# Kernel tuning notes

Hardware: AMD Instinct MI355X
Metric: run time of the kernel (lower is better)

Reference implementation:

```python
import jax, jax.numpy as jnp
import numpy as np

B, N, D, FF, L = 32, 1000, 128, 512, 6
EPS = 1e-5  # InstanceNorm1d default eps


def _inorm(x, g, b):
    # InstanceNorm1d on [B, d, N] == normalize over sequence dim N per channel (biased var)
    m = jnp.mean(x, axis=1, keepdims=True)
    v = jnp.var(x, axis=1, keepdims=True)
    return (x - m) / jnp.sqrt(v + EPS) * g + b


def setup_inputs() -> dict:
    key = jax.random.key(0)
    ks = jax.random.split(key, 10)
    s = 0.05
    data = jax.random.normal(ks[0], (B, N, 2), dtype=jnp.float32)
    # negative pairwise distances (module calls it negative_dist)
    dist = -jax.random.uniform(ks[1], (B, N, N), dtype=jnp.float32)
    log_scale = jnp.ones((1,), dtype=jnp.float32)
    We = jax.random.normal(ks[2], (D, 2), dtype=jnp.float32) * s
    be = jnp.zeros((D,), dtype=jnp.float32)
    Wq = jax.random.normal(ks[3], (L, D, D), dtype=jnp.float32) * s
    Wk = jax.random.normal(ks[4], (L, D, D), dtype=jnp.float32) * s
    Wv = jax.random.normal(ks[5], (L, D, D), dtype=jnp.float32) * s
    g1 = jnp.ones((L, D), dtype=jnp.float32)
    b1 = jnp.zeros((L, D), dtype=jnp.float32)
    W1 = jax.random.normal(ks[6], (L, FF, D), dtype=jnp.float32) * s
    bw1 = jnp.zeros((L, FF), dtype=jnp.float32)
    W2 = jax.random.normal(ks[7], (L, D, FF), dtype=jnp.float32) * s
    bw2 = jnp.zeros((L, D), dtype=jnp.float32)
    g2 = jnp.ones((L, D), dtype=jnp.float32)
    b2 = jnp.zeros((L, D), dtype=jnp.float32)
    alpha = jnp.ones((L,), dtype=jnp.float32)  # AFT_dist_alpha per layer
    return dict(data=data, dist=dist, log_scale=log_scale, We=We, be=be,
                Wq=Wq, Wk=Wk, Wv=Wv, g1=g1, b1=b1, W1=W1, bw1=bw1,
                W2=W2, bw2=bw2, g2=g2, b2=b2, alpha=alpha)


def reference(data, dist, log_scale, We, be, Wq, Wk, Wv, g1, b1, W1, bw1, W2, bw2, g2, b2, alpha):
    x = data @ We.T + be  # [B,N,D]
    for i in range(L):
        q = x @ Wq[i].T
        k = x @ Wk[i].T
        v = x @ Wv[i].T
        A = jnp.exp(log_scale[0] * alpha[i] * dist)  # [B,N,N]
        ek = jnp.exp(k)
        bias = jnp.einsum('bnm,bmd->bnd', A, ek * v)
        denom = jnp.einsum('bnm,bmd->bnd', A, ek)
        out = jax.nn.sigmoid(q) * (bias / denom)
        x1 = _inorm(x + out, g1[i], b1[i])
        h = jax.nn.relu(x1 @ W1[i].T + bw1[i]) @ W2[i].T + bw2[i]
        x = _inorm(x1 + h, g2[i], b2[i])
    return x
```

## Files before the change

kernel.cpp:

```cpp
#include <hip/hip_runtime.h>
#include <hip/hip_bf16.h>

typedef __attribute__((ext_vector_type(4))) float f32x4;
typedef __attribute__((ext_vector_type(8))) short bf16x8;
typedef __attribute__((ext_vector_type(4))) short s16x4;

#define LCOUNT 6

static __device__ __forceinline__ unsigned short f2b(float f){
  __hip_bfloat16 h = __float2bfloat16(f);
  return __builtin_bit_cast(unsigned short, h);
}
static __device__ __forceinline__ float b2f(unsigned short u){
  unsigned int x = ((unsigned int)u) << 16;
  return __builtin_bit_cast(float, x);
}
static __device__ __forceinline__ void gl16(const void* g, void* l){
  __builtin_amdgcn_global_load_lds(
      (const __attribute__((address_space(1))) void*)g,
      (__attribute__((address_space(3))) void*)l, 16, 0, 0);
}
static __device__ __forceinline__ f32x4 mfma16(bf16x8 a, bf16x8 b, f32x4 c){
  return __builtin_amdgcn_mfma_f32_16x16x32_bf16(a, b, c, 0, 0, 0);
}

__global__ void k_cvt5(const float* __restrict__ Wq, const float* __restrict__ Wk,
                       const float* __restrict__ Wv, const float* __restrict__ W1,
                       const float* __restrict__ W2,
                       unsigned short* __restrict__ wqb, unsigned short* __restrict__ wkb,
                       unsigned short* __restrict__ wvb, unsigned short* __restrict__ w1b,
                       unsigned short* __restrict__ w2b){
  int i = blockIdx.x*256 + threadIdx.x;
  if (i < 98304) wqb[i] = f2b(Wq[i]);
  else if (i < 196608) wkb[i-98304] = f2b(Wk[i-98304]);
  else if (i < 294912) wvb[i-196608] = f2b(Wv[i-196608]);
  else if (i < 688128) w1b[i-294912] = f2b(W1[i-294912]);
  else w2b[i-688128] = f2b(W2[i-688128]);
}

__global__ void k_cvtdist(const float* __restrict__ dist, unsigned short* __restrict__ db){
  int t = blockIdx.x*256 + threadIdx.x;
  int row = t >> 7, ch = t & 127;
  bf16x8 w;
  if (ch >= 125){
#pragma unroll
    for (int e=0;e<8;e++) w[e] = 0;
  } else {
    const float* p = dist + (size_t)row*1000 + ch*8;
    f32x4 a = *(const f32x4*)p;
    f32x4 b = *(const f32x4*)(p + 4);
#pragma unroll
    for (int e=0;e<4;e++){ w[e] = (short)f2b(a[e]); w[4+e] = (short)f2b(b[e]); }
  }
  *(bf16x8*)&db[(size_t)row*1024 + ch*8] = w;
}

__global__ void k_embed(const float* __restrict__ data, const float* __restrict__ We,
                        const float* __restrict__ be, float* __restrict__ x,
                        unsigned short* __restrict__ xb){
  int idx = blockIdx.x*256 + threadIdx.x;
  int d = idx & 127, bn = idx >> 7;
  float v = data[bn*2]*We[d*2] + data[bn*2+1]*We[d*2+1] + be[d];
  x[idx] = v; xb[idx] = f2b(v);
}

__global__ __launch_bounds__(256) void k_napply(
  const float* __restrict__ src, const float* __restrict__ part, int cnt,
  const float* __restrict__ g, const float* __restrict__ beta,
  float* __restrict__ dstf, unsigned short* __restrict__ dstb,
  float* __restrict__ dout)
{
  __shared__ float sna[128], snc[128];
  int blk = blockIdx.x, tid = threadIdx.x;
  int b = blk / 125;
  if (tid < 128){
    float s1 = 0.f, s2 = 0.f;
    for (int c = 0; c < cnt; ++c){
      size_t pi = (((size_t)b*cnt + c)*128 + tid)*2;
      s1 += part[pi]; s2 += part[pi+1];
    }
    float mean = s1 * 1e-3f;
    float var  = s2 * 1e-3f - mean*mean;
    float a = g[tid] * rsqrtf(var + 1e-5f);
    sna[tid] = a; snc[tid] = beta[tid] - mean*a;
  }
  __syncthreads();
  size_t base = (size_t)blk*1024 + tid*4;
  f32x4 v = *(const f32x4*)&src[base];
  int d0 = (tid*4) & 127;
  f32x4 o; s16x4 ob;
#pragma unroll
  for (int e=0;e<4;e++){
    o[e] = v[e]*sna[d0+e] + snc[d0+e];
    ob[e] = (short)f2b(o[e]);
  }
  *(f32x4*)&dstf[base] = o;
  *(s16x4*)&dstb[base] = ob;
  if (dout) *(f32x4*)&dout[base] = o;
}

__global__ __launch_bounds__(256) void k_qkv(
  const unsigned short* __restrict__ xb,
  const unsigned short* __restrict__ Wqb, const unsigned short* __restrict__ Wkb,
  const unsigned short* __restrict__ Wvb,
  unsigned short* __restrict__ sigq, unsigned short* __restrict__ Zc)
{
  __shared__ unsigned short LA[2][4][64][8];
  __shared__ unsigned short LB[2][4][256][8];
  int tid = threadIdx.x, wid = tid>>6, lane = tid&63;
  int l15 = lane&15, lg = lane>>4;
  int wm = wid>>1, wn = wid&1;
  int bt = blockIdx.x, b = bt>>4, t = bt&15;
  int kv = blockIdx.y;
  int lrow = t*64 + lane; if (lrow > 999) lrow = 999;
  size_t arow = (size_t)(b*1000 + lrow);

  f32x4 zf = {0.f,0.f,0.f,0.f};
  f32x4 acc[2][4], acc2[2][4];
#pragma unroll
  for (int i=0;i<2;i++)
#pragma unroll
    for (int j=0;j<4;j++){ acc[i][j] = zf; acc2[i][j] = zf; }

  auto stage = [&](int kk, int buf){
    int k0 = kk*32;
    gl16(xb + arow*128 + k0 + wid*8, &LA[buf][wid][0][0]);
    if (kv == 0){
#pragma unroll
      for (int t2=0;t2<2;++t2){
        int e = wid + t2*4, g2 = e>>1, nb = e&1;
        gl16(Wqb + (size_t)(nb*64+lane)*128 + k0 + g2*8, &LB[buf][g2][nb*64][0]);
      }
    } else {
#pragma unroll
      for (int t2=0;t2<4;++t2){
        int e = wid + t2*4, g2 = e&3, nb = e>>2;
        const unsigned short* src = (nb < 2)
          ? Wkb + (size_t)(nb*64+lane)*128 + k0 + g2*8
          : Wvb + (size_t)((nb-2)*64+lane)*128 + k0 + g2*8;
        gl16(src, &LB[buf][g2][nb*64][0]);
      }
    }
  };
  auto compute = [&](int buf){
    bf16x8 af[2];
#pragma unroll
    for (int i=0;i<2;i++) af[i] = *(const bf16x8*)&LA[buf][lg][wm*32 + i*16 + l15][0];
#pragma unroll
    for (int j=0;j<4;j++){
      bf16x8 bq = *(const bf16x8*)&LB[buf][lg][wn*64 + j*16 + l15][0];
#pragma unroll
      for (int i=0;i<2;i++) acc[i][j] = mfma16(af[i], bq, acc[i][j]);
      if (kv){
        bf16x8 bv = *(const bf16x8*)&LB[buf][lg][128 + wn*64 + j*16 + l15][0];
#pragma unroll
        for (int i=0;i<2;i++) acc2[i][j] = mfma16(af[i], bv, acc2[i][j]);
      }
    }
  };

  stage(0, 0);
  __syncthreads();
  for (int kk = 0; kk < 4; ++kk){
    int buf = kk & 1;
    if (kk < 3) stage(kk+1, buf^1);
    compute(buf);
    __syncthreads();
  }

#pragma unroll
  for (int i=0;i<2;i++){
    int m4 = t*64 + wm*32 + i*16 + lg*4;
    if (m4 >= 1000) continue;
#pragma unroll
    for (int j=0;j<4;j++){
      int col = wn*64 + j*16 + l15;
      if (kv == 0){
#pragma unroll
        for (int r=0;r<4;r++)
          sigq[(size_t)(b*1000 + m4 + r)*128 + col] = f2b(1.f/(1.f + __expf(-acc[i][j][r])));
      } else {
        s16x4 pv, pk;
#pragma unroll
        for (int r=0;r<4;r++){
          float ek = __expf(acc[i][j][r]);
          pk[r] = (short)f2b(ek);
          pv[r] = (short)f2b(ek * acc2[i][j][r]);
        }
        size_t base = ((size_t)(b*128 + (m4>>3))*256 + col)*8 + ((m4>>2)&1)*4;
        *(s16x4*)&Zc[base] = pv;
        *(s16x4*)&Zc[base + 1024] = pk;
      }
    }
  }
}

template<int USE16>
__global__ __launch_bounds__(256) void k_attn(
  const float* __restrict__ dist, const unsigned short* __restrict__ db16,
  const unsigned short* __restrict__ Zc, const unsigned short* __restrict__ sigq,
  float* __restrict__ x, float* __restrict__ partA,
  const float* __restrict__ log_scale, const float* __restrict__ alpha, int layer)
{
  union SM {
    struct { unsigned short A[2][4][32][8]; unsigned short B[2][4][256][8]; } st;
    float den[32][128];
  };
  __shared__ SM sm;
  int tid = threadIdx.x, wid = tid>>6, lane = tid&63;
  int l15 = lane&15, lg = lane>>4;
  int bb = blockIdx.y, t = blockIdx.x, n0 = t*32;
  float sc = log_scale[0]*alpha[layer];
  const unsigned short* Zb = Zc + ((size_t)bb << 18);
  int arow = (tid>>2)&31, ag = tid&3;
  int an = n0 + arow; if (an > 999) an = 999;
  const size_t drow = (size_t)(bb*1000 + an);

  f32x4 zf = {0.f,0.f,0.f,0.f};
  f32x4 acc[2][4];
#pragma unroll
  for (int i=0;i<2;i++)
#pragma unroll
    for (int j=0;j<4;j++) acc[i][j] = zf;

  auto issueB = [&](int kk, int buf){
#pragma unroll
    for (int t2=0;t2<4;++t2){
      int e = wid + t2*4, g2 = e&3, cb = e>>2;
      gl16(Zb + ((size_t)((kk*4 + g2)*256 + cb*64 + lane))*8, &sm.st.B[buf][g2][cb*64][0]);
    }
  };
  auto loadA = [&](int kk, float* v){
    int k0 = kk*32 + ag*8;
    if (USE16){
      bf16x8 r = *(const bf16x8*)(db16 + drow*1024 + k0);
#pragma unroll
      for (int e=0;e<8;e++) v[e] = b2f((unsigned short)r[e]);
    } else {
      const float* dp = dist + (size_t)drow*1000;
      if (k0 + 8 <= 1000){
        f32x4 a0 = *(const f32x4*)(dp + k0);
        f32x4 a1 = *(const f32x4*)(dp + k0 + 4);
#pragma unroll
        for (int e=0;e<4;e++){ v[e] = a0[e]; v[4+e] = a1[e]; }
      } else {
#pragma unroll
        for (int e=0;e<8;e++){
          int m = k0 + e; if (m > 999) m = 999;
          v[e] = dp[m];
        }
      }
    }
  };
  auto expwrite = [&](const float* v, int buf){
    bf16x8 w;
#pragma unroll
    for (int e=0;e<8;e++) w[e] = (short)f2b(__expf(sc*v[e]));
    *(bf16x8*)&sm.st.A[buf][ag][arow][0] = w;
  };
  auto compute = [&](int buf){
    bf16x8 af[2], bq[4];
#pragma unroll
    for (int i=0;i<2;i++) af[i] = *(const bf16x8*)&sm.st.A[buf][lg][i*16 + l15][0];
#pragma unroll
    for (int j=0;j<4;j++) bq[j] = *(const bf16x8*)&sm.st.B[buf][lg][wid*64 + j*16 + l15][0];
#pragma unroll
    for (int i=0;i<2;i++)
#pragma unroll
      for (int j=0;j<4;j++)
        acc[i][j] = mfma16(af[i], bq[j], acc[i][j]);
  };

  float av[8];
  issueB(0, 0);
  if (tid < 128) loadA(0, av);
  if (tid < 128) expwrite(av, 0);
  __syncthreads();
  for (int kk = 0; kk < 32; ++kk){
    int buf = kk & 1;
    float nv[8];
    if (kk < 31){
      issueB(kk+1, buf^1);
      if (tid < 128) loadA(kk+1, nv);
    }
    compute(buf);
    if (kk < 31 && tid < 128) expwrite(nv, buf^1);
    __syncthreads();
  }

  if (wid >= 2){
#pragma unroll
    for (int i=0;i<2;i++)
#pragma unroll
      for (int j=0;j<4;j++){
        int dcol = (wid-2)*64 + j*16 + l15;
#pragma unroll
        for (int r=0;r<4;r++)
          sm.den[i*16 + lg*4 + r][dcol] = acc[i][j][r];
      }
  }
  __syncthreads();
  if (wid < 2){
    float s1[4] = {0.f,0.f,0.f,0.f}, s2[4] = {0.f,0.f,0.f,0.f};
#pragma unroll
    for (int i=0;i<2;i++){
#pragma unroll
      for (int r=0;r<4;r++){
        int n = n0 + i*16 + lg*4 + r;
        if (n < 1000){
          size_t rowi = ((size_t)bb*1000 + n)*128;
#pragma unroll
          for (int j=0;j<4;j++){
            int d = wid*64 + j*16 + l15;
            float y = x[rowi + d] +
                      b2f(sigq[rowi + d]) * acc[i][j][r] / sm.den[i*16 + lg*4 + r][d];
            x[rowi + d] = y;
            s1[j] += y; s2[j] += y*y;
          }
        }
      }
    }
#pragma unroll
    for (int j=0;j<4;j++){
      s1[j] += __shfl_xor(s1[j], 16); s2[j] += __shfl_xor(s2[j], 16);
      s1[j] += __shfl_xor(s1[j], 32); s2[j] += __shfl_xor(s2[j], 32);
    }
    if (lg == 0){
#pragma unroll
      for (int j=0;j<4;j++){
        int d = wid*64 + j*16 + l15;
        size_t pi = (((size_t)bb*32 + t)*128 + d)*2;
        partA[pi] = s1[j]; partA[pi+1] = s2[j];
      }
    }
  }
}

__global__ __launch_bounds__(512) void k_ff1(
  const float* __restrict__ x, const float* __restrict__ partA,
  const float* __restrict__ g1, const float* __restrict__ b1,
  const unsigned short* __restrict__ W1b, const float* __restrict__ bw1,
  unsigned short* __restrict__ x1b, unsigned short* __restrict__ h1)
{
  __shared__ unsigned short LA[2][4][64][8];
  __shared__ unsigned short LB[2][4][512][8];
  __shared__ float sna[128], snc[128];
  int tid = threadIdx.x, wid = tid>>6, lane = tid&63;
  int l15 = lane&15, lg = lane>>4;
  int wm = wid>>2, wn = wid&3;
  int bt = blockIdx.x, b = bt>>4, t = bt&15;

  if (tid < 128){
    float s1 = 0.f, s2 = 0.f;
    for (int c = 0; c < 32; ++c){
      size_t pi = (((size_t)b*32 + c)*128 + tid)*2;
      s1 += partA[pi]; s2 += partA[pi+1];
    }
    float mean = s1 * 1e-3f;
    float var  = s2 * 1e-3f - mean*mean;
    float a = g1[tid] * rsqrtf(var + 1e-5f);
    sna[tid] = a; snc[tid] = b1[tid] - mean*a;
  }
  __syncthreads();

  f32x4 zf = {0.f,0.f,0.f,0.f};
  f32x4 acc[2][8];
#pragma unroll
  for (int i=0;i<2;i++)
#pragma unroll
    for (int j=0;j<8;j++) acc[i][j] = zf;

  auto stage = [&](int kk, int buf){
    int k0 = kk*32;
    if (tid < 256){
      int row = tid>>2, g2 = tid&3;
      int lr = t*64 + row;
      int rr = lr > 999 ? 999 : lr;
      const float* p = x + ((size_t)(b*1000 + rr))*128 + k0 + g2*8;
      f32x4 v0 = *(const f32x4*)p;
      f32x4 v1 = *(const f32x4*)(p + 4);
      bf16x8 w;
#pragma unroll
      for (int e=0;e<4;e++){
        int k = k0 + g2*8;
        w[e]   = (short)f2b(v0[e]*sna[k+e]   + snc[k+e]);
        w[4+e] = (short)f2b(v1[e]*sna[k+4+e] + snc[k+4+e]);
      }
      *(bf16x8*)&LA[buf][g2][row][0] = w;
      if (lr < 1000)
        *(bf16x8*)&x1b[((size_t)(b*1000 + lr))*128 + k0 + g2*8] = w;
    }
#pragma unroll
    for (int t2=0;t2<4;++t2){
      int e = wid*4 + t2;
      int g2 = e & 3, nb = e >> 2;
      gl16(W1b + (size_t)(nb*64 + lane)*128 + k0 + g2*8, &LB[buf][g2][nb*64][0]);
    }
  };
  auto compute = [&](int buf){
    bf16x8 af[2];
#pragma unroll
    for (int i=0;i<2;i++) af[i] = *(const bf16x8*)&LA[buf][lg][wm*32 + i*16 + l15][0];
#pragma unroll
    for (int j=0;j<8;j++){
      bf16x8 bq = *(const bf16x8*)&LB[buf][lg][wn*128 + j*16 + l15][0];
#pragma unroll
      for (int i=0;i<2;i++) acc[i][j] = mfma16(af[i], bq, acc[i][j]);
    }
  };

  stage(0, 0);
  __syncthreads();
  for (int kk = 0; kk < 4; ++kk){
    int buf = kk & 1;
    if (kk < 3) stage(kk+1, buf^1);
    compute(buf);
    __syncthreads();
  }

#pragma unroll
  for (int i=0;i<2;i++){
    int m4 = t*64 + wm*32 + i*16 + lg*4;
    if (m4 >= 1000) continue;
#pragma unroll
    for (int j=0;j<8;j++){
      int col = wn*128 + j*16 + l15;
      float bz = bw1[col];
#pragma unroll
      for (int r=0;r<4;r++){
        float v = acc[i][j][r] + bz;
        h1[(size_t)(b*1000 + m4 + r)*512 + col] = f2b(v > 0.f ? v : 0.f);
      }
    }
  }
}

__global__ __launch_bounds__(256) void k_ff2(
  const unsigned short* __restrict__ h1, const unsigned short* __restrict__ W2b,
  const float* __restrict__ bw2, const unsigned short* __restrict__ x1b,
  float* __restrict__ x, float* __restrict__ partF)
{
  __shared__ unsigned short LA[2][4][64][8];
  __shared__ unsigned short LB[2][4][128][8];
  int tid = threadIdx.x, wid = tid>>6, lane = tid&63;
  int l15 = lane&15, lg = lane>>4;
  int wm = wid>>1, wn = wid&1;
  int bt = blockIdx.x, b = bt>>4, t = bt&15;
  int lrow = t*64 + lane; if (lrow > 999) lrow = 999;
  size_t arow = (size_t)(b*1000 + lrow);

  f32x4 zf = {0.f,0.f,0.f,0.f};
  f32x4 acc[2][4];
#pragma unroll
  for (int i=0;i<2;i++)
#pragma unroll
    for (int j=0;j<4;j++) acc[i][j] = zf;

  auto stage = [&](int kk, int buf){
    int k0 = kk*32;
    gl16(h1 + arow*512 + k0 + wid*8, &LA[buf][wid][0][0]);
#pragma unroll
    for (int t2=0;t2<2;++t2){
      int e = wid + t2*4, g2 = e>>1, nb = e&1;
      gl16(W2b + (size_t)(nb*64 + lane)*512 + k0 + g2*8, &LB[buf][g2][nb*64][0]);
    }
  };
  auto compute = [&](int buf){
    bf16x8 af[2];
#pragma unroll
    for (int i=0;i<2;i++) af[i] = *(const bf16x8*)&LA[buf][lg][wm*32 + i*16 + l15][0];
#pragma unroll
    for (int j=0;j<4;j++){
      bf16x8 bq = *(const bf16x8*)&LB[buf][lg][wn*64 + j*16 + l15][0];
#pragma unroll
      for (int i=0;i<2;i++) acc[i][j] = mfma16(af[i], bq, acc[i][j]);
    }
  };

  stage(0, 0);
  __syncthreads();
  for (int kk = 0; kk < 16; ++kk){
    int buf = kk & 1;
    if (kk < 15) stage(kk+1, buf^1);
    compute(buf);
    __syncthreads();
  }

  float s1[4] = {0.f,0.f,0.f,0.f}, s2[4] = {0.f,0.f,0.f,0.f};
#pragma unroll
  for (int i=0;i<2;i++){
    int m4 = t*64 + wm*32 + i*16 + lg*4;
    if (m4 >= 1000) continue;
#pragma unroll
    for (int j=0;j<4;j++){
      int col = wn*64 + j*16 + l15;
      float bz = bw2[col];
#pragma unroll
      for (int r=0;r<4;r++){
        size_t idx = (size_t)(b*1000 + m4 + r)*128 + col;
        float y = acc[i][j][r] + bz + b2f(x1b[idx]);
        x[idx] = y;
        s1[j] += y; s2[j] += y*y;
      }
    }
  }
#pragma unroll
  for (int j=0;j<4;j++){
    s1[j] += __shfl_xor(s1[j], 16); s2[j] += __shfl_xor(s2[j], 16);
    s1[j] += __shfl_xor(s1[j], 32); s2[j] += __shfl_xor(s2[j], 32);
  }
  if (lg == 0){
#pragma unroll
    for (int j=0;j<4;j++){
      int d = wn*64 + j*16 + l15;
      size_t pi = (((size_t)b*32 + t*2 + wm)*128 + d)*2;
      partF[pi] = s1[j]; partF[pi+1] = s2[j];
    }
  }
}

extern "C" void kernel_launch(void* const* d_in, const int* in_sizes, int n_in,
                              void* d_out, int out_size, void* d_ws, size_t ws_size,
                              hipStream_t stream) {
  const float* data = (const float*)d_in[0];
  const float* dist = (const float*)d_in[1];
  const float* log_scale = (const float*)d_in[2];
  const float* We = (const float*)d_in[3];
  const float* be = (const float*)d_in[4];
  const float* Wq = (const float*)d_in[5];
  const float* Wk = (const float*)d_in[6];
  const float* Wv = (const float*)d_in[7];
  const float* g1 = (const float*)d_in[8];
  const float* b1 = (const float*)d_in[9];
  const float* W1 = (const float*)d_in[10];
  const float* bw1 = (const float*)d_in[11];
  const float* W2 = (const float*)d_in[12];
  const float* bw2 = (const float*)d_in[13];
  const float* g2 = (const float*)d_in[14];
  const float* b2 = (const float*)d_in[15];
  const float* alpha = (const float*)d_in[16];
  float* dout = (float*)d_out;

  char* ws = (char*)d_ws;
  size_t off = 0;
  auto alloc = [&](size_t bytes) -> void* {
    void* p = ws + off; off += (bytes + 255) & ~(size_t)255; return p;
  };
  unsigned short* xb  = (unsigned short*)alloc(8192000);
  float* x            = (float*)alloc(16384000);
  unsigned short* sigq= (unsigned short*)alloc(8192000);
  unsigned short* Zc  = (unsigned short*)alloc(16777216);
  unsigned short* h1  = (unsigned short*)alloc(32768000);
  unsigned short* x1b = (unsigned short*)alloc(8192000);
  float* partA        = (float*)alloc(1048576);
  float* partF        = (float*)alloc(1048576);
  unsigned short* wqb = (unsigned short*)alloc(196608);
  unsigned short* wkb = (unsigned short*)alloc(196608);
  unsigned short* wvb = (unsigned short*)alloc(196608);
  unsigned short* w1b = (unsigned short*)alloc(786432);
  unsigned short* w2b = (unsigned short*)alloc(786432);
  if (off > ws_size) return;
  unsigned short* db16p = nullptr;
  if (ws_size >= off + 131072256) db16p = (unsigned short*)alloc(131072000);

  hipMemsetAsync(Zc, 0, 16777216, stream);
  k_cvt5<<<4224, 256, 0, stream>>>(Wq, Wk, Wv, W1, W2, wqb, wkb, wvb, w1b, w2b);
  if (db16p) k_cvtdist<<<16000, 256, 0, stream>>>(dist, db16p);
  k_embed<<<16000, 256, 0, stream>>>(data, We, be, x, xb);

  for (int i = 0; i < LCOUNT; ++i){
    k_qkv<<<dim3(512,2), 256, 0, stream>>>(xb, wqb + i*16384, wkb + i*16384,
                                           wvb + i*16384, sigq, Zc);
    if (db16p)
      k_attn<1><<<dim3(32,32), 256, 0, stream>>>(dist, db16p, Zc, sigq, x, partA,
                                                 log_scale, alpha, i);
    else
      k_attn<0><<<dim3(32,32), 256, 0, stream>>>(dist, nullptr, Zc, sigq, x, partA,
                                                 log_scale, alpha, i);
    k_ff1<<<512, 512, 0, stream>>>(x, partA, g1 + i*128, b1 + i*128,
                                   w1b + i*65536, bw1 + i*512, x1b, h1);
    k_ff2<<<512, 256, 0, stream>>>(h1, w2b + i*65536, bw2 + i*128, x1b, x, partF);
    k_napply<<<4000, 256, 0, stream>>>(x, partF, 32, g2 + i*128, b2 + i*128,
                                       x, xb, (i == LCOUNT-1) ? dout : nullptr);
  }
}
```

Baseline: 927.7 us.

## Fuse second instance-norm apply into next layer's QKV and attention kernels

```diff
diff --git a/kernel.cpp b/kernel.cpp
--- a/kernel.cpp
+++ b/kernel.cpp
@@ -64,49 +64,46 @@
   x[idx] = v; xb[idx] = f2b(v);
 }
 
-__global__ __launch_bounds__(256) void k_napply(
-  const float* __restrict__ src, const float* __restrict__ part, int cnt,
-  const float* __restrict__ g, const float* __restrict__ beta,
-  float* __restrict__ dstf, unsigned short* __restrict__ dstb,
-  float* __restrict__ dout)
-{
-  __shared__ float sna[128], snc[128];
+__global__ void k_scale(const float* __restrict__ part, int cnt,
+                        const float* __restrict__ g, const float* __restrict__ beta,
+                        float* __restrict__ na, float* __restrict__ nc){
+  int b = blockIdx.x, d = threadIdx.x;
+  float s1 = 0.f, s2 = 0.f;
+  for (int c = 0; c < cnt; ++c){
+    size_t pi = (((size_t)b*cnt + c)*128 + d)*2;
+    s1 += part[pi]; s2 += part[pi+1];
+  }
+  float mean = s1 * 1e-3f;
+  float var  = s2 * 1e-3f - mean*mean;
+  float a = g[d] * rsqrtf(var + 1e-5f);
+  na[b*128 + d] = a; nc[b*128 + d] = beta[d] - mean*a;
+}
+
+__global__ __launch_bounds__(256) void k_fapply(
+  const float* __restrict__ x, const float* __restrict__ na,
+  const float* __restrict__ nc, float* __restrict__ dout){
   int blk = blockIdx.x, tid = threadIdx.x;
   int b = blk / 125;
-  if (tid < 128){
-    float s1 = 0.f, s2 = 0.f;
-    for (int c = 0; c < cnt; ++c){
-      size_t pi = (((size_t)b*cnt + c)*128 + tid)*2;
-      s1 += part[pi]; s2 += part[pi+1];
-    }
-    float mean = s1 * 1e-3f;
-    float var  = s2 * 1e-3f - mean*mean;
-    float a = g[tid] * rsqrtf(var + 1e-5f);
-    sna[tid] = a; snc[tid] = beta[tid] - mean*a;
-  }
-  __syncthreads();
   size_t base = (size_t)blk*1024 + tid*4;
-  f32x4 v = *(const f32x4*)&src[base];
   int d0 = (tid*4) & 127;
-  f32x4 o; s16x4 ob;
-#pragma unroll
-  for (int e=0;e<4;e++){
-    o[e] = v[e]*sna[d0+e] + snc[d0+e];
-    ob[e] = (short)f2b(o[e]);
-  }
-  *(f32x4*)&dstf[base] = o;
-  *(s16x4*)&dstb[base] = ob;
-  if (dout) *(f32x4*)&dout[base] = o;
-}
-
+  f32x4 v = *(const f32x4*)&x[base];
+  f32x4 o;
+#pragma unroll
+  for (int e=0;e<4;e++) o[e] = v[e]*na[b*128 + d0 + e] + nc[b*128 + d0 + e];
+  *(f32x4*)&dout[base] = o;
+}
+
+template<int NORM>
 __global__ __launch_bounds__(256) void k_qkv(
-  const unsigned short* __restrict__ xb,
+  const unsigned short* __restrict__ xb, const float* __restrict__ x,
+  const float* __restrict__ na2, const float* __restrict__ nc2,
   const unsigned short* __restrict__ Wqb, const unsigned short* __restrict__ Wkb,
   const unsigned short* __restrict__ Wvb,
   unsigned short* __restrict__ sigq, unsigned short* __restrict__ Zc)
 {
-  __shared__ unsigned short LA[2][4][64][8];
+  __shared__ unsigned short LA[2*2048];
   __shared__ unsigned short LB[2][4][256][8];
+  __shared__ float sna[128], snc[128];
   int tid = threadIdx.x, wid = tid>>6, lane = tid&63;
   int l15 = lane&15, lg = lane>>4;
   int wm = wid>>1, wn = wid&1;
@@ -115,6 +112,11 @@
   int lrow = t*64 + lane; if (lrow > 999) lrow = 999;
   size_t arow = (size_t)(b*1000 + lrow);
 
+  if (NORM){
+    if (tid < 128){ sna[tid] = na2[b*128 + tid]; snc[tid] = nc2[b*128 + tid]; }
+    __syncthreads();
+  }
+
   f32x4 zf = {0.f,0.f,0.f,0.f};
   f32x4 acc[2][4], acc2[2][4];
 #pragma unroll
@@ -124,7 +126,23 @@
 
   auto stage = [&](int kk, int buf){
     int k0 = kk*32;
-    gl16(xb + arow*128 + k0 + wid*8, &LA[buf][wid][0][0]);
+    if (NORM){
+      int row = tid>>2, g2 = tid&3;
+      int lr = t*64 + row; int rr = lr > 999 ? 999 : lr;
+      const float* p = x + ((size_t)(b*1000 + rr))*128 + k0 + g2*8;
+      f32x4 v0 = *(const f32x4*)p;
+      f32x4 v1 = *(const f32x4*)(p + 4);
+      bf16x8 w;
+#pragma unroll
+      for (int e=0;e<4;e++){
+        int k = k0 + g2*8;
+        w[e]   = (short)f2b(v0[e]*sna[k+e]   + snc[k+e]);
+        w[4+e] = (short)f2b(v1[e]*sna[k+4+e] + snc[k+4+e]);
+      }
+      *(bf16x8*)&LA[buf*2048 + row*32 + g2*8] = w;
+    } else {
+      gl16(xb + arow*128 + k0 + wid*8, &LA[buf*2048 + wid*512]);
+    }
     if (kv == 0){
 #pragma unroll
       for (int t2=0;t2<2;++t2){
@@ -145,7 +163,11 @@
   auto compute = [&](int buf){
     bf16x8 af[2];
 #pragma unroll
-    for (int i=0;i<2;i++) af[i] = *(const bf16x8*)&LA[buf][lg][wm*32 + i*16 + l15][0];
+    for (int i=0;i<2;i++){
+      int row = wm*32 + i*16 + l15;
+      af[i] = NORM ? *(const bf16x8*)&LA[buf*2048 + row*32 + lg*8]
+                   : *(const bf16x8*)&LA[buf*2048 + lg*512 + row*8];
+    }
 #pragma unroll
     for (int j=0;j<4;j++){
       bf16x8 bq = *(const bf16x8*)&LB[buf][lg][wn*64 + j*16 + l15][0];
@@ -195,31 +217,32 @@
   }
 }
 
-template<int USE16>
+template<int NORM, int USE16>
 __global__ __launch_bounds__(256) void k_attn(
   const float* __restrict__ dist, const unsigned short* __restrict__ db16,
   const unsigned short* __restrict__ Zc, const unsigned short* __restrict__ sigq,
   float* __restrict__ x, float* __restrict__ partA,
+  const float* __restrict__ na2, const float* __restrict__ nc2,
   const float* __restrict__ log_scale, const float* __restrict__ alpha, int layer)
 {
   union SM {
-    struct { unsigned short A[2][4][32][8]; unsigned short B[2][4][256][8]; } st;
-    float den[32][128];
+    struct { unsigned short A[2][64][4][8]; unsigned short B[2][4][256][8]; } st;
+    float den[64][128];
   };
   __shared__ SM sm;
   int tid = threadIdx.x, wid = tid>>6, lane = tid&63;
   int l15 = lane&15, lg = lane>>4;
-  int bb = blockIdx.y, t = blockIdx.x, n0 = t*32;
+  int bb = blockIdx.y, t = blockIdx.x, n0 = t*64;
   float sc = log_scale[0]*alpha[layer];
   const unsigned short* Zb = Zc + ((size_t)bb << 18);
-  int arow = (tid>>2)&31, ag = tid&3;
+  int arow = tid>>2, ag = tid&3;
   int an = n0 + arow; if (an > 999) an = 999;
   const size_t drow = (size_t)(bb*1000 + an);
 
   f32x4 zf = {0.f,0.f,0.f,0.f};
-  f32x4 acc[2][4];
-#pragma unroll
-  for (int i=0;i<2;i++)
+  f32x4 acc[4][4];
+#pragma unroll
+  for (int i=0;i<4;i++)
 #pragma unroll
     for (int j=0;j<4;j++) acc[i][j] = zf;
 
@@ -237,7 +260,7 @@
 #pragma unroll
       for (int e=0;e<8;e++) v[e] = b2f((unsigned short)r[e]);
     } else {
-      const float* dp = dist + (size_t)drow*1000;
+      const float* dp = dist + drow*1000;
       if (k0 + 8 <= 1000){
         f32x4 a0 = *(const f32x4*)(dp + k0);
         f32x4 a1 = *(const f32x4*)(dp + k0 + 4);
@@ -256,16 +279,16 @@
     bf16x8 w;
 #pragma unroll
     for (int e=0;e<8;e++) w[e] = (short)f2b(__expf(sc*v[e]));
-    *(bf16x8*)&sm.st.A[buf][ag][arow][0] = w;
+    *(bf16x8*)&sm.st.A[buf][arow][ag][0] = w;
   };
   auto compute = [&](int buf){
-    bf16x8 af[2], bq[4];
-#pragma unroll
-    for (int i=0;i<2;i++) af[i] = *(const bf16x8*)&sm.st.A[buf][lg][i*16 + l15][0];
+    bf16x8 af[4], bq[4];
+#pragma unroll
+    for (int i=0;i<4;i++) af[i] = *(const bf16x8*)&sm.st.A[buf][i*16 + l15][lg][0];
 #pragma unroll
     for (int j=0;j<4;j++) bq[j] = *(const bf16x8*)&sm.st.B[buf][lg][wid*64 + j*16 + l15][0];
 #pragma unroll
-    for (int i=0;i<2;i++)
+    for (int i=0;i<4;i++)
 #pragma unroll
       for (int j=0;j<4;j++)
         acc[i][j] = mfma16(af[i], bq[j], acc[i][j]);
@@ -273,24 +296,21 @@
 
   float av[8];
   issueB(0, 0);
-  if (tid < 128) loadA(0, av);
-  if (tid < 128) expwrite(av, 0);
+  loadA(0, av);
+  expwrite(av, 0);
   __syncthreads();
   for (int kk = 0; kk < 32; ++kk){
     int buf = kk & 1;
     float nv[8];
-    if (kk < 31){
-      issueB(kk+1, buf^1);
-      if (tid < 128) loadA(kk+1, nv);
-    }
+    if (kk < 31){ issueB(kk+1, buf^1); loadA(kk+1, nv); }
     compute(buf);
-    if (kk < 31 && tid < 128) expwrite(nv, buf^1);
+    if (kk < 31) expwrite(nv, buf^1);
     __syncthreads();
   }
 
   if (wid >= 2){
 #pragma unroll
-    for (int i=0;i<2;i++)
+    for (int i=0;i<4;i++)
 #pragma unroll
       for (int j=0;j<4;j++){
         int dcol = (wid-2)*64 + j*16 + l15;
@@ -301,9 +321,17 @@
   }
   __syncthreads();
   if (wid < 2){
+    float nav[4], ncv[4];
+    if (NORM){
+#pragma unroll
+      for (int j=0;j<4;j++){
+        int d = wid*64 + j*16 + l15;
+        nav[j] = na2[bb*128 + d]; ncv[j] = nc2[bb*128 + d];
+      }
+    }
     float s1[4] = {0.f,0.f,0.f,0.f}, s2[4] = {0.f,0.f,0.f,0.f};
 #pragma unroll
-    for (int i=0;i<2;i++){
+    for (int i=0;i<4;i++){
 #pragma unroll
       for (int r=0;r<4;r++){
         int n = n0 + i*16 + lg*4 + r;
@@ -312,8 +340,9 @@
 #pragma unroll
           for (int j=0;j<4;j++){
             int d = wid*64 + j*16 + l15;
-            float y = x[rowi + d] +
-                      b2f(sigq[rowi + d]) * acc[i][j][r] / sm.den[i*16 + lg*4 + r][d];
+            float xv = x[rowi + d];
+            if (NORM) xv = xv*nav[j] + ncv[j];
+            float y = xv + b2f(sigq[rowi + d]) * acc[i][j][r] / sm.den[i*16 + lg*4 + r][d];
             x[rowi + d] = y;
             s1[j] += y; s2[j] += y*y;
           }
@@ -329,7 +358,7 @@
 #pragma unroll
       for (int j=0;j<4;j++){
         int d = wid*64 + j*16 + l15;
-        size_t pi = (((size_t)bb*32 + t)*128 + d)*2;
+        size_t pi = (((size_t)bb*16 + t)*128 + d)*2;
         partA[pi] = s1[j]; partA[pi+1] = s2[j];
       }
     }
@@ -340,9 +369,9 @@
   const float* __restrict__ x, const float* __restrict__ partA,
   const float* __restrict__ g1, const float* __restrict__ b1,
   const unsigned short* __restrict__ W1b, const float* __restrict__ bw1,
-  unsigned short* __restrict__ x1b, unsigned short* __restrict__ h1)
+  float* __restrict__ x1, unsigned short* __restrict__ h1)
 {
-  __shared__ unsigned short LA[2][4][64][8];
+  __shared__ unsigned short LA[2][64][4][8];
   __shared__ unsigned short LB[2][4][512][8];
   __shared__ float sna[128], snc[128];
   int tid = threadIdx.x, wid = tid>>6, lane = tid&63;
@@ -352,8 +381,8 @@
 
   if (tid < 128){
     float s1 = 0.f, s2 = 0.f;
-    for (int c = 0; c < 32; ++c){
-      size_t pi = (((size_t)b*32 + c)*128 + tid)*2;
+    for (int c = 0; c < 16; ++c){
+      size_t pi = (((size_t)b*16 + c)*128 + tid)*2;
       s1 += partA[pi]; s2 += partA[pi+1];
     }
     float mean = s1 * 1e-3f;
@@ -379,16 +408,21 @@
       const float* p = x + ((size_t)(b*1000 + rr))*128 + k0 + g2*8;
       f32x4 v0 = *(const f32x4*)p;
       f32x4 v1 = *(const f32x4*)(p + 4);
+      f32x4 o0, o1;
       bf16x8 w;
 #pragma unroll
       for (int e=0;e<4;e++){
         int k = k0 + g2*8;
-        w[e]   = (short)f2b(v0[e]*sna[k+e]   + snc[k+e]);
-        w[4+e] = (short)f2b(v1[e]*sna[k+4+e] + snc[k+4+e]);
-      }
-      *(bf16x8*)&LA[buf][g2][row][0] = w;
-      if (lr < 1000)
-        *(bf16x8*)&x1b[((size_t)(b*1000 + lr))*128 + k0 + g2*8] = w;
+        o0[e] = v0[e]*sna[k+e]   + snc[k+e];
+        o1[e] = v1[e]*sna[k+4+e] + snc[k+4+e];
+        w[e]   = (short)f2b(o0[e]);
+        w[4+e] = (short)f2b(o1[e]);
+      }
+      *(bf16x8*)&LA[buf][row][g2][0] = w;
+      if (lr < 1000){
+        float* q = x1 + ((size_t)(b*1000 + lr))*128 + k0 + g2*8;
+        *(f32x4*)q = o0; *(f32x4*)(q+4) = o1;
+      }
     }
 #pragma unroll
     for (int t2=0;t2<4;++t2){
@@ -400,7 +434,7 @@
   auto compute = [&](int buf){
     bf16x8 af[2];
 #pragma unroll
-    for (int i=0;i<2;i++) af[i] = *(const bf16x8*)&LA[buf][lg][wm*32 + i*16 + l15][0];
+    for (int i=0;i<2;i++) af[i] = *(const bf16x8*)&LA[buf][wm*32 + i*16 + l15][lg][0];
 #pragma unroll
     for (int j=0;j<8;j++){
       bf16x8 bq = *(const bf16x8*)&LB[buf][lg][wn*128 + j*16 + l15][0];
@@ -437,7 +471,7 @@
 
 __global__ __launch_bounds__(256) void k_ff2(
   const unsigned short* __restrict__ h1, const unsigned short* __restrict__ W2b,
-  const float* __restrict__ bw2, const unsigned short* __restrict__ x1b,
+  const float* __restrict__ bw2, const float* __restrict__ x1,
   float* __restrict__ x, float* __restrict__ partF)
 {
   __shared__ unsigned short LA[2][4][64][8];
@@ -498,7 +532,7 @@
 #pragma unroll
       for (int r=0;r<4;r++){
         size_t idx = (size_t)(b*1000 + m4 + r)*128 + col;
-        float y = acc[i][j][r] + bz + b2f(x1b[idx]);
+        float y = acc[i][j][r] + bz + x1[idx];
         x[idx] = y;
         s1[j] += y; s2[j] += y*y;
       }
@@ -551,9 +585,11 @@
   unsigned short* sigq= (unsigned short*)alloc(8192000);
   unsigned short* Zc  = (unsigned short*)alloc(16777216);
   unsigned short* h1  = (unsigned short*)alloc(32768000);
-  unsigned short* x1b = (unsigned short*)alloc(8192000);
-  float* partA        = (float*)alloc(1048576);
+  float* x1           = (float*)alloc(16384000);
+  float* partA        = (float*)alloc(524288);
   float* partF        = (float*)alloc(1048576);
+  float* na2          = (float*)alloc(16384);
+  float* nc2          = (float*)alloc(16384);
   unsigned short* wqb = (unsigned short*)alloc(196608);
   unsigned short* wkb = (unsigned short*)alloc(196608);
   unsigned short* wvb = (unsigned short*)alloc(196608);
@@ -569,18 +605,31 @@
   k_embed<<<16000, 256, 0, stream>>>(data, We, be, x, xb);
 
   for (int i = 0; i < LCOUNT; ++i){
-    k_qkv<<<dim3(512,2), 256, 0, stream>>>(xb, wqb + i*16384, wkb + i*16384,
-                                           wvb + i*16384, sigq, Zc);
-    if (db16p)
-      k_attn<1><<<dim3(32,32), 256, 0, stream>>>(dist, db16p, Zc, sigq, x, partA,
-                                                 log_scale, alpha, i);
+    if (i > 0)
+      k_scale<<<32, 128, 0, stream>>>(partF, 32, g2 + (i-1)*128, b2 + (i-1)*128, na2, nc2);
+    if (i == 0)
+      k_qkv<0><<<dim3(512,2), 256, 0, stream>>>(xb, x, nullptr, nullptr,
+                                                wqb + i*16384, wkb + i*16384, wvb + i*16384,
+                                                sigq, Zc);
     else
-      k_attn<0><<<dim3(32,32), 256, 0, stream>>>(dist, nullptr, Zc, sigq, x, partA,
-                                                 log_scale, alpha, i);
+      k_qkv<1><<<dim3(512,2), 256, 0, stream>>>(nullptr, x, na2, nc2,
+                                                wqb + i*16384, wkb + i*16384, wvb + i*16384,
+                                                sigq, Zc);
+    if (i == 0){
+      if (db16p) k_attn<0,1><<<dim3(16,32), 256, 0, stream>>>(dist, db16p, Zc, sigq, x, partA,
+                                                              nullptr, nullptr, log_scale, alpha, i);
+      else       k_attn<0,0><<<dim3(16,32), 256, 0, stream>>>(dist, nullptr, Zc, sigq, x, partA,
+                                                              nullptr, nullptr, log_scale, alpha, i);
+    } else {
+      if (db16p) k_attn<1,1><<<dim3(16,32), 256, 0, stream>>>(dist, db16p, Zc, sigq, x, partA,
+                                                              na2, nc2, log_scale, alpha, i);
+      else       k_attn<1,0><<<dim3(16,32), 256, 0, stream>>>(dist, nullptr, Zc, sigq, x, partA,
+                                                              na2, nc2, log_scale, alpha, i);
+    }
     k_ff1<<<512, 512, 0, stream>>>(x, partA, g1 + i*128, b1 + i*128,
-                                   w1b + i*65536, bw1 + i*512, x1b, h1);
-    k_ff2<<<512, 256, 0, stream>>>(h1, w2b + i*65536, bw2 + i*128, x1b, x, partF);
-    k_napply<<<4000, 256, 0, stream>>>(x, partF, 32, g2 + i*128, b2 + i*128,
-                                       x, xb, (i == LCOUNT-1) ? dout : nullptr);
-  }
-}
+                                   w1b + i*65536, bw1 + i*512, x1, h1);
+    k_ff2<<<512, 256, 0, stream>>>(h1, w2b + i*65536, bw2 + i*128, x1, x, partF);
+  }
+  k_scale<<<32, 128, 0, stream>>>(partF, 32, g2 + 5*128, b2 + 5*128, na2, nc2);
+  k_fapply<<<4000, 256, 0, stream>>>(x, na2, nc2, dout);
+}
```

Measured after the change: 858.1 us. 1.08x faster.
